# Optimization experiments

Hardware: AMD Instinct MI355X
Metric: run time of the kernel (lower is better)

Reference implementation:

```python
import jax, jax.numpy as jnp
import numpy as np

N_PATCH = 4194304  # H*W with H=W=2048
H_GT, W_GT = 2050, 2050  # gt padded by 1 on each side


def setup_inputs() -> dict:
    key = jax.random.key(0)
    k1, k2, k3 = jax.random.split(key, 3)
    image = jax.random.uniform(k1, (N_PATCH, 3, 3), dtype=jnp.float32)
    edges_prob = jax.random.uniform(k2, (N_PATCH, 3, 3), dtype=jnp.float32)
    gt = jax.random.uniform(k3, (H_GT, W_GT), dtype=jnp.float32)
    return {"image": image, "edges_prob": edges_prob, "gt": gt}


def reference(image, edges_prob, gt):
    # image: [N,3,3], edges_prob: [N,3,3], gt: [H+2, W+2]
    N = image.shape[0]
    img = image.reshape(N, 9)
    edg = edges_prob.reshape(N, 9)

    # Per-patch segment reduce: edg==0 -> ignored; edg>0.5 -> disacc; else -> acc
    m_dis = edg > 0.5
    m_acc = (edg != 0.0) & ~m_dis
    c_dis = m_dis.sum(axis=-1)
    c_acc = m_acc.sum(axis=-1)
    md = (img * m_dis).sum(axis=-1) / jnp.maximum(c_dis, 1)  # mean of disacc group
    ma = (img * m_acc).sum(axis=-1) / jnp.maximum(c_acc, 1)  # mean of acc group
    valid = (c_dis > 0) & (c_acc > 0)

    # 0 = black, 1 = white, 2 = unknown
    out = jnp.where(valid, jnp.where(md > ma, 0.0, 1.0), 2.0)

    # Global masked means of center pixels over black / white classes
    values = image[:, 1, 1]
    mb = (out == 0.0)
    mw = (out == 1.0)
    avgB = (values * mb).sum() / jnp.maximum(mb.sum(), 1)
    avgW = (values * mw).sum() / jnp.maximum(mw.sum(), 1)

    # Correction: resolve unknowns by nearest class average
    corr = jnp.where(
        out == 2.0,
        jnp.where(jnp.abs(values - avgB) < jnp.abs(values - avgW), 0.0, 1.0),
        out,
    )

    H = gt.shape[0] - 2
    W = gt.shape[1] - 2
    return corr.reshape(H, W)
```

## Files before the change

### kernel.cpp

```cpp
#include <hip/hip_runtime.h>


struct Partial { float sb, sw; unsigned int cb, cw; };
struct Acc     { double sumB, sumW; unsigned int cntB, cntW; };

#define NBLK1   4096
#define CHUNKS  4
#define LCAP    64
#define PART_OFF 0
#define ACC_OFF  (NBLK1 * 16)
#define CNT_OFF  (ACC_OFF + 64)
#define ENT_OFF  (CNT_OFF + NBLK1 * 4)
#define WS_NEED  (ENT_OFF + NBLK1 * LCAP * 4)

__device__ __forceinline__ int classify(const float* ip, const float* ep, float& value) {
    float xd[9], xa[9];
    int cd = 0, ca = 0;
#pragma unroll
    for (int k = 0; k < 9; ++k) {
        float e = ep[k], v = ip[k];
        bool dis = e > 0.5f;
        bool ac  = (e != 0.0f) && !dis;
        xd[k] = dis ? v : 0.0f;
        xa[k] = ac  ? v : 0.0f;
        cd += dis ? 1 : 0;
        ca += ac  ? 1 : 0;
    }
    float sd = ((xd[0] + xd[1]) + (xd[2] + xd[3])) + ((xd[4] + xd[5]) + (xd[6] + xd[7]));
    sd += xd[8];
    float sa = ((xa[0] + xa[1]) + (xa[2] + xa[3])) + ((xa[4] + xa[5]) + (xa[6] + xa[7]));
    sa += xa[8];
    const int cdm = cd > 0 ? cd : 1;
    const int cam = ca > 0 ? ca : 1;
    const bool gt = ((double)sd * (double)cam) > ((double)sa * (double)cdm);
    value = ip[4];
    return (cd > 0 && ca > 0) ? (gt ? 0 : 1) : 2;
}

__global__ __launch_bounds__(256) void phase1(const float* __restrict__ img,
                                              const float* __restrict__ edg,
                                              float* __restrict__ out,
                                              Partial* __restrict__ part,
                                              unsigned int* __restrict__ cnts,
                                              unsigned int* __restrict__ ents,
                                              int useList)
{
    __shared__ float s_img[256 * 9];
    __shared__ float s_edg[256 * 9];
    __shared__ unsigned int slist[LCAP];
    __shared__ unsigned int s_cnt;
    const int t = threadIdx.x;
    if (t == 0) s_cnt = 0;

    float accB = 0.0f, accW = 0.0f;
    int   ncb = 0, ncw = 0;

    for (int c = 0; c < CHUNKS; ++c) {
        const size_t chunk = (size_t)blockIdx.x * CHUNKS + c;
        const size_t base  = chunk * (256 * 9);
        const float4* gi = reinterpret_cast<const float4*>(img + base);
        const float4* ge = reinterpret_cast<const float4*>(edg + base);
        float4* si = reinterpret_cast<float4*>(s_img);
        float4* se = reinterpret_cast<float4*>(s_edg);
        si[t]       = gi[t];       se[t]       = ge[t];
        si[t + 256] = gi[t + 256]; se[t + 256] = ge[t + 256];
        if (t < 64) { si[t + 512] = gi[t + 512]; se[t + 512] = ge[t + 512]; }
        __syncthreads();

        float v;
        int code = classify(s_img + 9 * t, s_edg + 9 * t, v);
        out[chunk * 256 + t] = (float)code;
        accB += (code == 0) ? v : 0.0f;
        accW += (code == 1) ? v : 0.0f;
        ncb  += (code == 0) ? 1 : 0;
        ncw  += (code == 1) ? 1 : 0;

        if (useList) {
            const unsigned long long m2 = __ballot(code == 2);
            const int lane = t & 63;
            unsigned int wbase = 0;
            if (lane == 0 && m2)
                wbase = atomicAdd(&s_cnt, (unsigned)__popcll(m2));
            wbase = __shfl(wbase, 0);
            if (code == 2) {
                const unsigned pos = wbase + (unsigned)__popcll(m2 & ((1ull << lane) - 1ull));
                if (pos < LCAP) slist[pos] = (unsigned)(chunk * 256 + t);
            }
        }
        __syncthreads();
    }

#pragma unroll
    for (int off = 32; off > 0; off >>= 1) {
        accB += __shfl_down(accB, off);
        accW += __shfl_down(accW, off);
        ncb  += __shfl_down(ncb, off);
        ncw  += __shfl_down(ncw, off);
    }
    __shared__ float rb[4], rw[4];
    __shared__ unsigned int ub[4], uw[4];
    const int wave = t >> 6, lane = t & 63;
    if (lane == 0) { rb[wave] = accB; rw[wave] = accW; ub[wave] = ncb; uw[wave] = ncw; }
    __syncthreads();
    if (t == 0) {
        Partial p;
        p.sb = (rb[0] + rb[1]) + (rb[2] + rb[3]);
        p.sw = (rw[0] + rw[1]) + (rw[2] + rw[3]);
        p.cb = ub[0] + ub[1] + ub[2] + ub[3];
        p.cw = uw[0] + uw[1] + uw[2] + uw[3];
        part[blockIdx.x] = p;
    }
    if (useList) {
        const unsigned int n = s_cnt < LCAP ? s_cnt : LCAP;
        if (t == 0) cnts[blockIdx.x] = n;
        if (t < n)  ents[(size_t)blockIdx.x * LCAP + t] = slist[t];
    }
}

__global__ __launch_bounds__(256) void reduceK(const Partial* __restrict__ part,
                                               int n, Acc* __restrict__ acc)
{
    const int t = threadIdx.x;
    double sb = 0.0, sw = 0.0;
    unsigned int cb = 0, cw = 0;
    for (int i = t; i < n; i += 256) {
        Partial p = part[i];
        sb += (double)p.sb; sw += (double)p.sw; cb += p.cb; cw += p.cw;
    }
#pragma unroll
    for (int off = 32; off > 0; off >>= 1) {
        sb += __shfl_down(sb, off);
        sw += __shfl_down(sw, off);
        cb += __shfl_down(cb, off);
        cw += __shfl_down(cw, off);
    }
    __shared__ double db[4], dw[4];
    __shared__ unsigned int eb[4], ew[4];
    const int wave = t >> 6, lane = t & 63;
    if (lane == 0) { db[wave] = sb; dw[wave] = sw; eb[wave] = cb; ew[wave] = cw; }
    __syncthreads();
    if (t == 0) {
        Acc a;
        a.sumB = db[0] + db[1] + db[2] + db[3];
        a.sumW = dw[0] + dw[1] + dw[2] + dw[3];
        a.cntB = eb[0] + eb[1] + eb[2] + eb[3];
        a.cntW = ew[0] + ew[1] + ew[2] + ew[3];
        *acc = a;
    }
}

__global__ __launch_bounds__(64) void phase2_list(const float* __restrict__ img,
                                                  float* __restrict__ out,
                                                  const Acc* __restrict__ acc,
                                                  const unsigned int* __restrict__ cnts,
                                                  const unsigned int* __restrict__ ents)
{
    const unsigned int n = cnts[blockIdx.x];
    if (threadIdx.x < n) {
        const unsigned cb = acc->cntB, cw = acc->cntW;
        const double avgB = acc->sumB / (double)(cb ? cb : 1u);
        const double avgW = acc->sumW / (double)(cw ? cw : 1u);
        const unsigned int p = ents[(size_t)blockIdx.x * LCAP + threadIdx.x];
        const double v = (double)img[(size_t)p * 9 + 4];
        out[p] = (fabs(v - avgB) < fabs(v - avgW)) ? 0.0f : 1.0f;
    }
}

__global__ __launch_bounds__(256) void phase2_scan(const float* __restrict__ img,
                                                   float* __restrict__ out,
                                                   const Acc* __restrict__ acc,
                                                   int n4)
{
    const int i = blockIdx.x * 256 + threadIdx.x;
    if (i >= n4) return;
    float4 v = reinterpret_cast<const float4*>(out)[i];
    if (v.x == 2.0f || v.y == 2.0f || v.z == 2.0f || v.w == 2.0f) {
        const unsigned cb = acc->cntB, cw = acc->cntW;
        const double avgB = acc->sumB / (double)(cb ? cb : 1u);
        const double avgW = acc->sumW / (double)(cw ? cw : 1u);
        float r[4] = {v.x, v.y, v.z, v.w};
#pragma unroll
        for (int j = 0; j < 4; ++j) {
            if (r[j] == 2.0f) {
                const size_t p = (size_t)i * 4 + j;
                const double val = (double)img[p * 9 + 4];
                out[p] = (fabs(val - avgB) < fabs(val - avgW)) ? 0.0f : 1.0f;
            }
        }
    }
}

extern "C" void kernel_launch(void* const* d_in, const int* in_sizes, int n_in,
                              void* d_out, int out_size, void* d_ws, size_t ws_size,
                              hipStream_t stream) {
    const float* img = (const float*)d_in[0];
    const float* edg = (const float*)d_in[1];
    float* out = (float*)d_out;
    char* ws = (char*)d_ws;

    Partial*      part = (Partial*)(ws + PART_OFF);
    Acc*          acc  = (Acc*)(ws + ACC_OFF);
    unsigned int* cnts = (unsigned int*)(ws + CNT_OFF);
    unsigned int* ents = (unsigned int*)(ws + ENT_OFF);

    const int useList = (ws_size >= (size_t)WS_NEED) ? 1 : 0;
    const int N = in_sizes[0] / 9;

    phase1<<<NBLK1, 256, 0, stream>>>(img, edg, out, part, cnts, ents, useList);
    reduceK<<<1, 256, 0, stream>>>(part, NBLK1, acc);
    if (useList) {
        phase2_list<<<NBLK1, 64, 0, stream>>>(img, out, acc, cnts, ents);
    } else {
        const int n4 = N / 4;
        phase2_scan<<<(n4 + 255) / 256, 256, 0, stream>>>(img, out, acc, n4);
    }
}
```

Measured before the change: 67.01 us.

## Fuse global partial reduction into list-based correction kernel, dropping one launch

Removes the single-block reduceK launch on the list path. Each of 256 blocks of the new phase2 kernel redundantly reduces all 4096 per-block partials and then corrects 16 source blocks' unknown-pixel lists. This saves a kernel launch and its serialization gap. In exchange, every block re-reads the full partial array (64 KB each, 256 times), which adds L2 traffic.

```diff
diff --git a/kernel.cpp b/kernel.cpp
--- a/kernel.cpp
+++ b/kernel.cpp
@@ -7,6 +7,7 @@
 #define NBLK1   4096
 #define CHUNKS  4
 #define LCAP    64
+#define B2GRID  256
 #define PART_OFF 0
 #define ACC_OFF  (NBLK1 * 16)
 #define CNT_OFF  (ACC_OFF + 64)
@@ -117,14 +118,16 @@
     }
 }
 
-__global__ __launch_bounds__(256) void reduceK(const Partial* __restrict__ part,
-                                               int n, Acc* __restrict__ acc)
+__device__ __forceinline__ void reducePartials(const Partial* __restrict__ part,
+                                               double& sumB, double& sumW,
+                                               unsigned int& cntB, unsigned int& cntW)
 {
     const int t = threadIdx.x;
     double sb = 0.0, sw = 0.0;
     unsigned int cb = 0, cw = 0;
-    for (int i = t; i < n; i += 256) {
-        Partial p = part[i];
+#pragma unroll
+    for (int i = 0; i < NBLK1; i += 256) {
+        Partial p = part[i + t];
         sb += (double)p.sb; sw += (double)p.sw; cb += p.cb; cw += p.cw;
     }
 #pragma unroll
@@ -136,33 +139,57 @@
     }
     __shared__ double db[4], dw[4];
     __shared__ unsigned int eb[4], ew[4];
+    __shared__ double fb[2];
+    __shared__ unsigned int fc[2];
     const int wave = t >> 6, lane = t & 63;
     if (lane == 0) { db[wave] = sb; dw[wave] = sw; eb[wave] = cb; ew[wave] = cw; }
     __syncthreads();
     if (t == 0) {
-        Acc a;
-        a.sumB = db[0] + db[1] + db[2] + db[3];
-        a.sumW = dw[0] + dw[1] + dw[2] + dw[3];
-        a.cntB = eb[0] + eb[1] + eb[2] + eb[3];
-        a.cntW = ew[0] + ew[1] + ew[2] + ew[3];
+        fb[0] = db[0] + db[1] + db[2] + db[3];
+        fb[1] = dw[0] + dw[1] + dw[2] + dw[3];
+        fc[0] = eb[0] + eb[1] + eb[2] + eb[3];
+        fc[1] = ew[0] + ew[1] + ew[2] + ew[3];
+    }
+    __syncthreads();
+    sumB = fb[0]; sumW = fb[1]; cntB = fc[0]; cntW = fc[1];
+}
+
+__global__ __launch_bounds__(256) void phase2(const float* __restrict__ img,
+                                              float* __restrict__ out,
+                                              const Partial* __restrict__ part,
+                                              const unsigned int* __restrict__ cnts,
+                                              const unsigned int* __restrict__ ents)
+{
+    double sumB, sumW;
+    unsigned int cb, cw;
+    reducePartials(part, sumB, sumW, cb, cw);
+    const double avgB = sumB / (double)(cb ? cb : 1u);
+    const double avgW = sumW / (double)(cw ? cw : 1u);
+
+    const int t = threadIdx.x;
+    const int per = NBLK1 / B2GRID;
+#pragma unroll
+    for (int j = 0; j < per; ++j) {
+        const unsigned int b = blockIdx.x * per + j;
+        const unsigned int n = cnts[b];
+        if (t < (int)n) {
+            const unsigned int p = ents[(size_t)b * LCAP + t];
+            const double v = (double)img[(size_t)p * 9 + 4];
+            out[p] = (fabs(v - avgB) < fabs(v - avgW)) ? 0.0f : 1.0f;
+        }
+    }
+}
+
+
+__global__ __launch_bounds__(256) void reduceK(const Partial* __restrict__ part,
+                                               Acc* __restrict__ acc)
+{
+    double sumB, sumW;
+    unsigned int cb, cw;
+    reducePartials(part, sumB, sumW, cb, cw);
+    if (threadIdx.x == 0) {
+        Acc a; a.sumB = sumB; a.sumW = sumW; a.cntB = cb; a.cntW = cw;
         *acc = a;
-    }
-}
-
-__global__ __launch_bounds__(64) void phase2_list(const float* __restrict__ img,
-                                                  float* __restrict__ out,
-                                                  const Acc* __restrict__ acc,
-                                                  const unsigned int* __restrict__ cnts,
-                                                  const unsigned int* __restrict__ ents)
-{
-    const unsigned int n = cnts[blockIdx.x];
-    if (threadIdx.x < n) {
-        const unsigned cb = acc->cntB, cw = acc->cntW;
-        const double avgB = acc->sumB / (double)(cb ? cb : 1u);
-        const double avgW = acc->sumW / (double)(cw ? cw : 1u);
-        const unsigned int p = ents[(size_t)blockIdx.x * LCAP + threadIdx.x];
-        const double v = (double)img[(size_t)p * 9 + 4];
-        out[p] = (fabs(v - avgB) < fabs(v - avgW)) ? 0.0f : 1.0f;
     }
 }
 
@@ -207,10 +234,10 @@
     const int N = in_sizes[0] / 9;
 
     phase1<<<NBLK1, 256, 0, stream>>>(img, edg, out, part, cnts, ents, useList);
-    reduceK<<<1, 256, 0, stream>>>(part, NBLK1, acc);
     if (useList) {
-        phase2_list<<<NBLK1, 64, 0, stream>>>(img, out, acc, cnts, ents);
+        phase2<<<B2GRID, 256, 0, stream>>>(img, out, part, cnts, ents);
     } else {
+        reduceK<<<1, 256, 0, stream>>>(part, acc);
         const int n4 = N / 4;
         phase2_scan<<<(n4 + 255) / 256, 256, 0, stream>>>(img, out, acc, n4);
     }
```

Result: slower. 73.83 us (+10.2%).
